# Optimization experiments

Hardware: AMD Instinct MI355X
Metric: run time of the kernel (lower is better)

## Reference

```python
import jax, jax.numpy as jnp
import numpy as np

B, C, H, T = 512, 128, 128, 512


def setup_inputs() -> dict:
    key = jax.random.key(0)
    ks = jax.random.split(key, 9)
    s = 1.0 / np.sqrt(C + H)  # torch Linear default init scale
    u = lambda k, shape: jax.random.uniform(k, shape, jnp.float32, -s, s)
    return {
        "x": jax.random.normal(ks[0], (B, C, T), jnp.float32),
        "Wf": u(ks[1], (C + H, H)), "bf": u(ks[2], (H,)),
        "Wi": u(ks[3], (C + H, H)), "bi": u(ks[4], (H,)),
        "Wu": u(ks[5], (C + H, H)), "bu": u(ks[6], (H,)),
        "Wo": u(ks[7], (C + H, H)), "bo": u(ks[8], (H,)),
    }


def reference(x, Wf, bf, Wi, bi, Wu, bu, Wo, bo):
    # x: (B, C, T); scan over time with (h, c) carry. Single layer (num_layers=1).
    batch = x.shape[0]
    hid = Wf.shape[1]
    xT = jnp.moveaxis(x, -1, 0)  # (T, B, C)

    def step(carry, xt):
        h, c = carry
        s = jnp.concatenate([xt, h], axis=-1)  # (B, C+H)
        f = jax.nn.sigmoid(s @ Wf + bf)
        i = jax.nn.sigmoid(s @ Wi + bi)
        g = jnp.tanh(s @ Wu + bu)
        o = jax.nn.sigmoid(s @ Wo + bo)
        c = c * f + i * g
        h = o * jnp.tanh(c)
        return (h, c), h

    h0 = jnp.zeros((batch, hid), x.dtype)
    (_, c_final), hs = jax.lax.scan(step, (h0, h0), xT)  # hs: (T, B, H)
    h_seq = jnp.moveaxis(hs, 0, -1)  # (B, H, T), matches torch stack(dim=-1)
    return h_seq, c_final
```

## Files before the change

### kernel.cpp

```cpp
#include <hip/hip_runtime.h>


#define BB 512
#define CC 128
#define HH 128
#define TT 512
#define MB 2
#define XSP 168
#define XZP 516
#define OPH 33

typedef __attribute__((ext_vector_type(8))) short short8;
typedef __attribute__((ext_vector_type(4))) float f32x4;
typedef __attribute__((ext_vector_type(2))) float f32x2;
typedef __attribute__((ext_vector_type(4))) int v4i;

#define SW 2032.0f
#define SH 127.0f
#define INV_SHW (1.0f / (127.0f * 2032.0f))

__device__ inline unsigned short f2bf(float f) {
    unsigned u = __builtin_bit_cast(unsigned, f);
    u = u + 0x7FFFu + ((u >> 16) & 1u);
    return (unsigned short)(u >> 16);
}
__device__ inline float bf2f(unsigned short s) {
    unsigned u = ((unsigned)s) << 16;
    return __builtin_bit_cast(float, u);
}

#define BAR() asm volatile("s_waitcnt lgkmcnt(0)\n\ts_barrier" ::: "memory")

__global__ __launch_bounds__(512, 2) void pclstm_kernel(
    const float* __restrict__ x,
    const float* __restrict__ Wf, const float* __restrict__ bfp,
    const float* __restrict__ Wi, const float* __restrict__ bip,
    const float* __restrict__ Wu, const float* __restrict__ bup,
    const float* __restrict__ Wo, const float* __restrict__ bop,
    float* __restrict__ out)
{
    __shared__ unsigned short xs[64][XSP];
    __shared__ signed char hs8[2][2][192];
    __shared__ float xz[2][16][XZP];
    __shared__ unsigned short hbuf[2][2][HH][OPH];

    const int tid  = threadIdx.x;
    const int lane = tid & 63;
    const int wid  = tid >> 6;
    const int bg0  = blockIdx.x * MB;
    const int l15  = lane & 15;
    const int q    = lane >> 4;
    const int qe   = q & 1;
    const int rb   = q >> 1;
    const int b4   = lane & 16;
    const int koff = q << 3;
    const int kq   = q << 4;
    const int un   = wid * 16 + l15;
    const int cqe  = (un << 2) + (qe << 1);

    const float esc_e = qe ? -2.885390082f : -1.442695041f;
    const float ym_e  = qe ? 2.0f : 1.0f;
    const float yk_e  = qe ? -1.0f : 0.0f;

    const float* Wg[4] = {Wf, Wi, Wu, Wo};
    const float* Bg[4] = {bfp, bip, bup, bop};
    short8 wx[4][4];
    v4i wh[4][2];
    float bias[4];
    #pragma unroll
    for (int g = 0; g < 4; ++g) {
        bias[g] = Bg[g][un];
        #pragma unroll
        for (int kt = 0; kt < 4; ++kt) {
            short8 v;
            #pragma unroll
            for (int i = 0; i < 8; ++i)
                v[i] = (short)f2bf(Wg[g][(kt * 32 + koff + i) * HH + un]);
            wx[g][kt] = v;
        }
        #pragma unroll
        for (int kf = 0; kf < 2; ++kf) {
            v4i v;
            #pragma unroll
            for (int d = 0; d < 4; ++d) {
                unsigned pw = 0;
                #pragma unroll
                for (int e = 0; e < 4; ++e) {
                    int qv = (int)__builtin_rintf(
                        Wg[g][(128 + kf * 64 + kq + d * 4 + e) * HH + un] * SW);
                    pw |= ((unsigned)(qv & 255)) << (8 * e);
                }
                v[d] = (int)pw;
            }
            wh[g][kf] = v;
        }
    }

    for (int i = tid; i < 2 * 2 * 192; i += 512)
        ((signed char*)hs8)[i] = 0;

    {
        int cc = (tid >> 2) & 127, sq0 = tid & 3;
        const float* xp = x + ((size_t)bg0 * CC + cc) * TT + sq0 * 4;
        f32x4 v0 = *(const f32x4*)xp;
        f32x4 v1 = *(const f32x4*)(xp + (size_t)CC * TT);
        #pragma unroll
        for (int j = 0; j < 4; ++j) {
            xs[2 * (sq0 * 4 + j) + 0][cc] = f2bf(v0[j]);
            xs[2 * (sq0 * 4 + j) + 1][cc] = f2bf(v1[j]);
        }
    }
    __syncthreads();

    auto xzg = [&](int TB) {
        const int buf = (TB >> 3) & 1;
        f32x4 a2[4];
        #pragma unroll
        for (int g = 0; g < 4; ++g)
            a2[g] = (f32x4){bias[g], bias[g], bias[g], bias[g]};
        #pragma unroll
        for (int kt = 0; kt < 4; ++kt) {
            const int s = (TB + (l15 >> 1)) & 31;
            short8 a = *(const short8*)&xs[2 * s + (lane & 1)][kt * 32 + koff];
            #pragma unroll
            for (int g = 0; g < 4; ++g)
                a2[g] = __builtin_amdgcn_mfma_f32_16x16x32_bf16(a, wx[g][kt], a2[g], 0, 0, 0);
        }
        const int row0 = q << 2;
        #pragma unroll
        for (int r = 0; r < 4; ++r) {
            f32x4 vv = {a2[0][r], a2[1][r], a2[2][r], a2[3][r]};
            *(f32x4*)&xz[buf][row0 + r][un << 2] = vv;
        }
    };

    xzg(0);
    __syncthreads();

    f32x2 nx = *(const f32x2*)&xz[0][rb][cqe];

    float cst = 0.0f;
    f32x4 stg0 = {0, 0, 0, 0}, stg1 = {0, 0, 0, 0};
    float* outH = out;
    float* outC = out + (size_t)BB * HH * TT;
    const int scc = (tid >> 2) & 127, sq = tid & 3;
    const int fb = tid >> 8, fn = (tid >> 1) & 127, fh = tid & 1;

    for (int t = 0; t < TT; ++t) {
        const int p = t & 1;
        v4i a0 = *(const v4i*)&hs8[p][lane & 1][kq];
        v4i a1 = *(const v4i*)&hs8[p][lane & 1][64 + kq];
        v4i zi[4];
        #pragma unroll
        for (int g = 0; g < 4; ++g) {
            v4i ac = {0, 0, 0, 0};
            ac = __builtin_amdgcn_mfma_i32_16x16x64_i8(a0, wh[g][0], ac, 0, 0, 0);
            zi[g] = __builtin_amdgcn_mfma_i32_16x16x64_i8(a1, wh[g][1], ac, 0, 0, 0);
        }

        const int tm = t & 15;
        if (tm == 0) {
            if (t + 16 < TT) {
                const float* xp = x + ((size_t)bg0 * CC + scc) * TT + (t + 16) + sq * 4;
                stg0 = *(const f32x4*)xp;
                stg1 = *(const f32x4*)(xp + (size_t)CC * TT);
            }
        } else if (tm == 8) {
            if (t + 8 < TT) {
                #pragma unroll
                for (int j = 0; j < 4; ++j) {
                    int sl = (t + 8 + sq * 4 + j) & 31;
                    xs[2 * sl + 0][scc] = f2bf(stg0[j]);
                    xs[2 * sl + 1][scc] = f2bf(stg1[j]);
                }
            }
        }
        if ((t & 7) == 1 && t + 7 < TT)
            xzg(t + 7);
        if ((t & 31) == 12 && t >= 32) {
            const int ocp = (t >> 5) - 1;
            const unsigned short* hb = &hbuf[ocp & 1][fb][fn][fh * 16];
            float* op = outH + ((size_t)(bg0 + fb) * HH + fn) * TT + ocp * 32 + fh * 16;
            f32x4 o[4];
            #pragma unroll
            for (int j = 0; j < 16; ++j)
                o[j >> 2][j & 3] = bf2f(hb[j]);
            #pragma unroll
            for (int qq = 0; qq < 4; ++qq)
                *(f32x4*)(op + 4 * qq) = o[qq];
        }

        {
            f32x2 xa = nx;
            {
                const int t1 = t + 1;
                const int buf1 = (t1 >> 3) & 1, dt1 = t1 & 7;
                nx = *(const f32x2*)&xz[buf1][2 * dt1 + rb][cqe];
            }
            int zf = rb ? zi[0][1] : zi[0][0];
            int zig = rb ? zi[1][1] : zi[1][0];
            int zu = rb ? zi[2][1] : zi[2][0];
            int zo = rb ? zi[3][1] : zi[3][0];
            int z_e = qe ? zu : zf;
            int z_o = qe ? zo : zig;
            float ze = (float)z_e * INV_SHW + xa.x;
            float zod = (float)z_o * INV_SHW + xa.y;
            float act_e = ym_e * __builtin_amdgcn_rcpf(
                              1.0f + __builtin_amdgcn_exp2f(esc_e * ze)) + yk_e;
            float act_o = __builtin_amdgcn_rcpf(
                              1.0f + __builtin_amdgcn_exp2f(-1.442695041f * zod));
            float cr_e = __shfl_xor(act_e, 16, 64);
            float cr_o = __shfl_xor(act_o, 16, 64);
            float fg = qe ? cr_e : act_e;
            float ig = qe ? cr_o : act_o;
            float ug = qe ? act_e : cr_e;
            float og = qe ? act_o : cr_o;
            cst = cst * fg + ig * ug;
            float th = 2.0f * __builtin_amdgcn_rcpf(
                           1.0f + __builtin_amdgcn_exp2f(-2.885390082f * cst)) - 1.0f;
            float h = og * th;
            if (!b4) {
                hs8[p ^ 1][rb][un] = (signed char)(int)__builtin_rintf(h * SH);
                hbuf[(t >> 5) & 1][rb][un][t & 31] = f2bf(h);
            }
        }
        BAR();
    }

    {
        const unsigned short* hb = &hbuf[1][fb][fn][fh * 16];
        float* op = outH + ((size_t)(bg0 + fb) * HH + fn) * TT + 480 + fh * 16;
        f32x4 o[4];
        #pragma unroll
        for (int j = 0; j < 16; ++j)
            o[j >> 2][j & 3] = bf2f(hb[j]);
        #pragma unroll
        for (int qq = 0; qq < 4; ++qq)
            *(f32x4*)(op + 4 * qq) = o[qq];
    }
    if (!b4)
        outC[(size_t)(bg0 + rb) * HH + un] = cst;
}

extern "C" void kernel_launch(void* const* d_in, const int* in_sizes, int n_in,
                              void* d_out, int out_size, void* d_ws, size_t ws_size,
                              hipStream_t stream) {
    const float* x  = (const float*)d_in[0];
    const float* Wf = (const float*)d_in[1];
    const float* bf = (const float*)d_in[2];
    const float* Wi = (const float*)d_in[3];
    const float* bi = (const float*)d_in[4];
    const float* Wu = (const float*)d_in[5];
    const float* bu = (const float*)d_in[6];
    const float* Wo = (const float*)d_in[7];
    const float* bo = (const float*)d_in[8];
    float* out = (float*)d_out;

    dim3 grid(BB / MB);
    dim3 block(512);
    pclstm_kernel<<<grid, block, 0, stream>>>(x, Wf, bf, Wi, bi, Wu, bu, Wo, bo, out);
}
```

Before: 311.2 us.

## Spread input projection over timesteps, split int8 MFMA chains, drop gate shuffles

The bf16 input-projection GEMM is no longer run as one burst every 8 steps. It is split into one k-tile per step across steps 1-4 of each 8-step phase, so its latency interleaves with the recurrent step. The two dependent int8 MFMAs per gate become independent MFMAs summed in scalar code, which shortens the dependency chain. Each lane now computes all four gate activations itself from an f32x4 load instead of two activations plus cross-lane shuffles. This adds transcendental work per lane and keeps the a2 accumulators live across iterations, which raises register pressure.

Result: slower. 582.9 us (+87.3%).

```diff
diff --git a/kernel.cpp b/kernel.cpp
--- a/kernel.cpp
+++ b/kernel.cpp
@@ -12,7 +12,6 @@
 
 typedef __attribute__((ext_vector_type(8))) short short8;
 typedef __attribute__((ext_vector_type(4))) float f32x4;
-typedef __attribute__((ext_vector_type(2))) float f32x2;
 typedef __attribute__((ext_vector_type(4))) int v4i;
 
 #define SW 2032.0f
@@ -50,17 +49,12 @@
     const int bg0  = blockIdx.x * MB;
     const int l15  = lane & 15;
     const int q    = lane >> 4;
-    const int qe   = q & 1;
     const int rb   = q >> 1;
     const int b4   = lane & 16;
     const int koff = q << 3;
     const int kq   = q << 4;
     const int un   = wid * 16 + l15;
-    const int cqe  = (un << 2) + (qe << 1);
-
-    const float esc_e = qe ? -2.885390082f : -1.442695041f;
-    const float ym_e  = qe ? 2.0f : 1.0f;
-    const float yk_e  = qe ? -1.0f : 0.0f;
+    const int cq4  = un << 2;
 
     const float* Wg[4] = {Wf, Wi, Wu, Wo};
     const float* Bg[4] = {bfp, bip, bup, bop};
@@ -112,32 +106,30 @@
     }
     __syncthreads();
 
-    auto xzg = [&](int TB) {
-        const int buf = (TB >> 3) & 1;
-        f32x4 a2[4];
+    f32x4 a2[4];
+
+    {
         #pragma unroll
         for (int g = 0; g < 4; ++g)
             a2[g] = (f32x4){bias[g], bias[g], bias[g], bias[g]};
         #pragma unroll
         for (int kt = 0; kt < 4; ++kt) {
-            const int s = (TB + (l15 >> 1)) & 31;
+            const int s = (l15 >> 1);
             short8 a = *(const short8*)&xs[2 * s + (lane & 1)][kt * 32 + koff];
             #pragma unroll
             for (int g = 0; g < 4; ++g)
                 a2[g] = __builtin_amdgcn_mfma_f32_16x16x32_bf16(a, wx[g][kt], a2[g], 0, 0, 0);
         }
-        const int row0 = q << 2;
+        const int r0 = q << 2;
         #pragma unroll
         for (int r = 0; r < 4; ++r) {
             f32x4 vv = {a2[0][r], a2[1][r], a2[2][r], a2[3][r]};
-            *(f32x4*)&xz[buf][row0 + r][un << 2] = vv;
-        }
-    };
-
-    xzg(0);
+            *(f32x4*)&xz[0][r0 + r][cq4] = vv;
+        }
+    }
     __syncthreads();
 
-    f32x2 nx = *(const f32x2*)&xz[0][rb][cqe];
+    f32x4 nx = *(const f32x4*)&xz[0][rb][cq4];
 
     float cst = 0.0f;
     f32x4 stg0 = {0, 0, 0, 0}, stg1 = {0, 0, 0, 0};
@@ -150,12 +142,12 @@
         const int p = t & 1;
         v4i a0 = *(const v4i*)&hs8[p][lane & 1][kq];
         v4i a1 = *(const v4i*)&hs8[p][lane & 1][64 + kq];
-        v4i zi[4];
+        v4i zi0[4], zi1[4];
+        const v4i zero4 = {0, 0, 0, 0};
         #pragma unroll
         for (int g = 0; g < 4; ++g) {
-            v4i ac = {0, 0, 0, 0};
-            ac = __builtin_amdgcn_mfma_i32_16x16x64_i8(a0, wh[g][0], ac, 0, 0, 0);
-            zi[g] = __builtin_amdgcn_mfma_i32_16x16x64_i8(a1, wh[g][1], ac, 0, 0, 0);
+            zi0[g] = __builtin_amdgcn_mfma_i32_16x16x64_i8(a0, wh[g][0], zero4, 0, 0, 0);
+            zi1[g] = __builtin_amdgcn_mfma_i32_16x16x64_i8(a1, wh[g][1], zero4, 0, 0, 0);
         }
 
         const int tm = t & 15;
@@ -175,8 +167,32 @@
                 }
             }
         }
-        if ((t & 7) == 1 && t + 7 < TT)
-            xzg(t + 7);
+        {
+            const int ph = t & 7;
+            const int TB = (t & ~7) + 8;
+            if (ph >= 1 && ph <= 4 && TB < TT) {
+                const int kt = ph - 1;
+                const int s = (TB + (l15 >> 1)) & 31;
+                short8 a = *(const short8*)&xs[2 * s + (lane & 1)][kt * 32 + koff];
+                if (kt == 0) {
+                    #pragma unroll
+                    for (int g = 0; g < 4; ++g)
+                        a2[g] = (f32x4){bias[g], bias[g], bias[g], bias[g]};
+                }
+                #pragma unroll
+                for (int g = 0; g < 4; ++g)
+                    a2[g] = __builtin_amdgcn_mfma_f32_16x16x32_bf16(a, wx[g][kt], a2[g], 0, 0, 0);
+                if (kt == 3) {
+                    const int bufw = (TB >> 3) & 1;
+                    const int r0 = q << 2;
+                    #pragma unroll
+                    for (int r = 0; r < 4; ++r) {
+                        f32x4 vv = {a2[0][r], a2[1][r], a2[2][r], a2[3][r]};
+                        *(f32x4*)&xz[bufw][r0 + r][cq4] = vv;
+                    }
+                }
+            }
+        }
         if ((t & 31) == 12 && t >= 32) {
             const int ocp = (t >> 5) - 1;
             const unsigned short* hb = &hbuf[ocp & 1][fb][fn][fh * 16];
@@ -191,30 +207,28 @@
         }
 
         {
-            f32x2 xa = nx;
+            f32x4 xa = nx;
             {
                 const int t1 = t + 1;
                 const int buf1 = (t1 >> 3) & 1, dt1 = t1 & 7;
-                nx = *(const f32x2*)&xz[buf1][2 * dt1 + rb][cqe];
-            }
-            int zf = rb ? zi[0][1] : zi[0][0];
-            int zig = rb ? zi[1][1] : zi[1][0];
-            int zu = rb ? zi[2][1] : zi[2][0];
-            int zo = rb ? zi[3][1] : zi[3][0];
-            int z_e = qe ? zu : zf;
-            int z_o = qe ? zo : zig;
-            float ze = (float)z_e * INV_SHW + xa.x;
-            float zod = (float)z_o * INV_SHW + xa.y;
-            float act_e = ym_e * __builtin_amdgcn_rcpf(
-                              1.0f + __builtin_amdgcn_exp2f(esc_e * ze)) + yk_e;
-            float act_o = __builtin_amdgcn_rcpf(
-                              1.0f + __builtin_amdgcn_exp2f(-1.442695041f * zod));
-            float cr_e = __shfl_xor(act_e, 16, 64);
-            float cr_o = __shfl_xor(act_o, 16, 64);
-            float fg = qe ? cr_e : act_e;
-            float ig = qe ? cr_o : act_o;
-            float ug = qe ? act_e : cr_e;
-            float og = qe ? act_o : cr_o;
+                nx = *(const f32x4*)&xz[buf1][2 * dt1 + rb][cq4];
+            }
+            int zf = (rb ? zi0[0][1] : zi0[0][0]) + (rb ? zi1[0][1] : zi1[0][0]);
+            int zg = (rb ? zi0[1][1] : zi0[1][0]) + (rb ? zi1[1][1] : zi1[1][0]);
+            int zu = (rb ? zi0[2][1] : zi0[2][0]) + (rb ? zi1[2][1] : zi1[2][0]);
+            int zo = (rb ? zi0[3][1] : zi0[3][0]) + (rb ? zi1[3][1] : zi1[3][0]);
+            float vf = (float)zf * INV_SHW + xa[0];
+            float vi = (float)zg * INV_SHW + xa[1];
+            float vu = (float)zu * INV_SHW + xa[2];
+            float vo = (float)zo * INV_SHW + xa[3];
+            float fg = __builtin_amdgcn_rcpf(
+                           1.0f + __builtin_amdgcn_exp2f(-1.442695041f * vf));
+            float ig = __builtin_amdgcn_rcpf(
+                           1.0f + __builtin_amdgcn_exp2f(-1.442695041f * vi));
+            float ug = 2.0f * __builtin_amdgcn_rcpf(
+                           1.0f + __builtin_amdgcn_exp2f(-2.885390082f * vu)) - 1.0f;
+            float og = __builtin_amdgcn_rcpf(
+                           1.0f + __builtin_amdgcn_exp2f(-1.442695041f * vo));
             cst = cst * fg + ig * ug;
             float th = 2.0f * __builtin_amdgcn_rcpf(
                            1.0f + __builtin_amdgcn_exp2f(-2.885390082f * cst)) - 1.0f;
```
